# Optimization experiments

Hardware: AMD Instinct MI355X
Metric: run time of the kernel (lower is better)

## Reference

```python
import jax, jax.numpy as jnp
import numpy as np

SCALE_DTYPE = jnp.float32

def rotate_half(x):
    half = x.shape[-1] // 2
    return jnp.concatenate([-x[..., half:], x[..., :half]], axis=-1)

def apply_rope(x, cos, sin):
    # x: [B,T,H,Dh]; cos/sin: [T,Dh] -> broadcast to [1,T,1,Dh]
    c = cos[None, :, None, :]
    s = sin[None, :, None, :]
    return x * c + rotate_half(x) * s

def setup_inputs() -> dict:
    key = jax.random.key(0)
    ks = jax.random.split(key, 7)
    B, T, D, H, Dh = 4, 2048, 1024, 16, 64
    x = jax.random.normal(ks[0], (B, T, D), dtype=jnp.float32)
    cos = jax.random.uniform(ks[1], (T, Dh), dtype=jnp.float32)
    sin = jax.random.uniform(ks[2], (T, Dh), dtype=jnp.float32)
    scale = 1.0 / np.sqrt(D)
    Wq = jax.random.normal(ks[3], (D, D), dtype=jnp.float32) * scale
    Wk = jax.random.normal(ks[4], (D, D), dtype=jnp.float32) * scale
    Wv = jax.random.normal(ks[5], (D, D), dtype=jnp.float32) * scale
    Wo = jax.random.normal(ks[6], (D, D), dtype=jnp.float32) * scale
    return {"x": x, "cos": cos, "sin": sin, "Wq": Wq, "Wk": Wk, "Wv": Wv, "Wo": Wo}

def reference(x, cos, sin, Wq, Wk, Wv, Wo):
    B, T, D = x.shape
    H, Dh = 16, 64
    # Linear projections (weights stored [in, out]) and split heads
    q = (x @ Wq).reshape(B, T, H, Dh)
    k = (x @ Wk).reshape(B, T, H, Dh)
    v = (x @ Wv).reshape(B, T, H, Dh)
    q = apply_rope(q, cos[:T], sin[:T])
    k = apply_rope(k, cos[:T], sin[:T])
    scale = 1.0 / jnp.sqrt(jnp.asarray(Dh, dtype=x.dtype))
    # [B,H,T,T] causal scores
    scores = jnp.einsum('bthd,bshd->bhts', q, k) * scale
    causal = jnp.tril(jnp.ones((T, T), dtype=bool))
    scores = jnp.where(causal[None, None, :, :], scores, jnp.asarray(-jnp.inf, dtype=scores.dtype))
    weights = jax.nn.softmax(scores, axis=-1)
    out = jnp.einsum('bhts,bshd->bthd', weights, v).reshape(B, T, D)
    return out @ Wo
```

## Files before the change

kernel.cpp:

```cpp
#include <hip/hip_runtime.h>
#include <cstdint>
#include <cstddef>

typedef unsigned short ushort_t;
typedef __attribute__((ext_vector_type(8))) short short8;
typedef __attribute__((ext_vector_type(4))) float float4v;
typedef __attribute__((ext_vector_type(4))) unsigned short ushort4v;

__device__ __forceinline__ float b2f(ushort_t u) {
    uint32_t x = ((uint32_t)u) << 16;
    float f;
    __builtin_memcpy(&f, &x, 4);
    return f;
}
__device__ __forceinline__ ushort_t f2b(float f) {
    uint32_t x;
    __builtin_memcpy(&x, &f, 4);
    uint32_t r = (x + 0x7fffu + ((x >> 16) & 1u)) >> 16;
    return (ushort_t)r;
}
__device__ __forceinline__ ushort_t f2b_trunc(float f) {
    uint32_t x;
    __builtin_memcpy(&x, &f, 4);
    return (ushort_t)(x >> 16);
}

typedef __attribute__((address_space(3))) void lds_void;
typedef __attribute__((address_space(1))) const void gbl_void;
__device__ __forceinline__ void gload16(const void* g, void* l) {
    __builtin_amdgcn_global_load_lds((gbl_void*)(uintptr_t)g, (lds_void*)(uintptr_t)l, 16, 0, 0);
}

__global__ void detect_dtype(const ushort_t* __restrict__ cosp, int* __restrict__ flag) {
    int tid = threadIdx.x;
    int bad = 0;
    for (int i = tid; i < 512; i += 64) {
        ushort_t u = cosp[i];
        int sign = u >> 15;
        int e = (u >> 7) & 0xFF;
        if (sign || e > 126) bad = 1;
    }
    int anybad = __any(bad);
    if (tid == 0) *flag = anybad ? 1 : 0;
}

__global__ __launch_bounds__(256) void convert_x(const void* __restrict__ in,
                                                 ushort_t* __restrict__ out,
                                                 const int* __restrict__ flag) {
    if (*flag == 0) return;
    int i = (blockIdx.x * 256 + threadIdx.x) * 4;
    float4v v = *(const float4v*)((const float*)in + i);
    ushort4v o;
#pragma unroll
    for (int j = 0; j < 4; ++j) o[j] = f2b(v[j]);
    *(ushort4v*)(out + i) = o;
}

__global__ __launch_bounds__(256) void convert_cs(const void* __restrict__ c,
                                                  const void* __restrict__ s,
                                                  ushort_t* __restrict__ cb,
                                                  ushort_t* __restrict__ sb,
                                                  const int* __restrict__ flag) {
    int f = *flag;
    int i = blockIdx.x * 256 + threadIdx.x;
    if (i >= 131072) return;
    if (f) {
        cb[i] = f2b(((const float*)c)[i]);
        sb[i] = f2b(((const float*)s)[i]);
    } else {
        cb[i] = ((const ushort_t*)c)[i];
        sb[i] = ((const ushort_t*)s)[i];
    }
}

__global__ __launch_bounds__(256) void transpose_w4(const void* __restrict__ w0,
                                                    const void* __restrict__ w1,
                                                    const void* __restrict__ w2,
                                                    const void* __restrict__ w3,
                                                    ushort_t* __restrict__ out,
                                                    const int* __restrict__ flag) {
    int f = *flag;
    int z = blockIdx.z;
    const void* in = (z == 0) ? w0 : (z == 1) ? w1 : (z == 2) ? w2 : w3;
    ushort_t* o = out + (size_t)z * 1024 * 1024;
    __shared__ ushort_t tile[32][33];
    int bx = blockIdx.x * 32;
    int by = blockIdx.y * 32;
    int tx = threadIdx.x & 31;
    int ty = threadIdx.x >> 5;
    for (int r = ty; r < 32; r += 8) {
        size_t idx = (size_t)(by + r) * 1024 + bx + tx;
        tile[r][tx] = f ? f2b(((const float*)in)[idx]) : ((const ushort_t*)in)[idx];
    }
    __syncthreads();
    for (int r = ty; r < 32; r += 8)
        o[(size_t)(bx + r) * 1024 + by + tx] = tile[tx][r];
}

template <int W>
__device__ __forceinline__ void vm_wait() {
    if constexpr (W == 6)      asm volatile("s_waitcnt vmcnt(6)" ::: "memory");
    else                       asm volatile("s_waitcnt vmcnt(0)" ::: "memory");
}
#define KBAR()                                       \
    do {                                             \
        asm volatile("" ::: "memory");               \
        __builtin_amdgcn_s_barrier();                \
        asm volatile("" ::: "memory");               \
    } while (0)

__global__ __launch_bounds__(512, 2) void gemm_qkv(const ushort_t* __restrict__ X0,
                                                   const ushort_t* __restrict__ X1,
                                                   const ushort_t* __restrict__ Wt,
                                                   ushort_t* __restrict__ qk,
                                                   ushort_t* __restrict__ vt,
                                                   const ushort_t* __restrict__ cosb,
                                                   const ushort_t* __restrict__ sinb,
                                                   const int* __restrict__ flagp) {
    __shared__ ushort_t LDS[73728];
    char* LDSc = (char*)LDS;

    int tid = threadIdx.x;
    int lane = tid & 63;
    int wave = tid >> 6;
    int wm = wave >> 1;
    int wn = wave & 1;
    int quad = lane >> 4;
    int l16 = lane & 15;

    int id = blockIdx.x;
    int xcd = id & 7;
    int r = id >> 3;
    int m0 = (r & 31) * 256;
    int n0 = (xcd * 3 + (r >> 5)) * 128;

    const ushort_t* Xb = (*flagp) ? X1 : X0;

    int lrow = lane >> 3;
    int lslot = (lane & 7) ^ lrow;
    const ushort_t* aSrc = Xb + (size_t)(m0 + wave * 32 + lrow) * 1024 + lslot * 8;
    const ushort_t* bSrc = Wt + (size_t)(n0 + wave * 16 + lrow) * 1024 + lslot * 8;
    int ldsA_w = (wave * 32) * 128;
    int ldsB_w = (wave * 16) * 128;

    int aoff0 = (wm * 64 + l16) * 128 + ((quad ^ (l16 & 7)) * 16);
    int aoff1 = (wm * 64 + l16) * 128 + (((4 + quad) ^ (l16 & 7)) * 16);
    int boff0 = (wn * 64 + l16) * 128 + ((quad ^ (l16 & 7)) * 16);
    int boff1 = (wn * 64 + l16) * 128 + (((4 + quad) ^ (l16 & 7)) * 16);

    float4v acc[4][4];
#pragma unroll
    for (int i = 0; i < 4; ++i)
#pragma unroll
        for (int n = 0; n < 4; ++n) acc[i][n] = (float4v){0.f, 0.f, 0.f, 0.f};

#define STAGE6(t, jj)                                                       \
    do {                                                                    \
        const ushort_t* as_ = aSrc + (jj) * 64;                             \
        const ushort_t* bs_ = bSrc + (jj) * 64;                             \
        char* al_ = LDSc + (t) * 32768 + ldsA_w;                            \
        char* bl_ = LDSc + 98304 + (t) * 16384 + ldsB_w;                    \
        gload16(as_, al_);                                                  \
        gload16(as_ + 8 * 1024, al_ + 1024);                                \
        gload16(as_ + 16 * 1024, al_ + 2048);                               \
        gload16(as_ + 24 * 1024, al_ + 3072);                               \
        gload16(bs_, bl_);                                                  \
        gload16(bs_ + 8 * 1024, bl_ + 1024);                                \
    } while (0)

#define COMPUTE(t)                                                          \
    do {                                                                    \
        const char* ab_ = LDSc + (t) * 32768;                               \
        const char* bb_ = LDSc + 98304 + (t) * 16384;                       \
        short8 a0_[4], b0_[4], a1_[4], b1_[4];                              \
        _Pragma("unroll") for (int i = 0; i < 4; ++i) {                     \
            a0_[i] = *(const short8*)(ab_ + aoff0 + i * 2048);              \
            a1_[i] = *(const short8*)(ab_ + aoff1 + i * 2048);              \
        }                                                                   \
        _Pragma("unroll") for (int n = 0; n < 4; ++n) {                     \
            b0_[n] = *(const short8*)(bb_ + boff0 + n * 2048);              \
            b1_[n] = *(const short8*)(bb_ + boff1 + n * 2048);              \
        }                                                                   \
        __builtin_amdgcn_s_setprio(1);                                      \
        _Pragma("unroll") for (int i = 0; i < 4; ++i)                       \
            _Pragma("unroll") for (int n = 0; n < 4; ++n)                   \
                acc[i][n] = __builtin_amdgcn_mfma_f32_16x16x32_bf16(        \
                    a0_[i], b0_[n], acc[i][n], 0, 0, 0);                    \
        _Pragma("unroll") for (int i = 0; i < 4; ++i)                       \
            _Pragma("unroll") for (int n = 0; n < 4; ++n)                   \
                acc[i][n] = __builtin_amdgcn_mfma_f32_16x16x32_bf16(        \
                    a1_[i], b1_[n], acc[i][n], 0, 0, 0);                    \
        __builtin_amdgcn_s_setprio(0);                                      \
    } while (0)

    STAGE6(0, 0);
    STAGE6(1, 1);
    vm_wait<6>();
    KBAR();

#pragma unroll 1
    for (int g = 0; g < 4; ++g) {
        int j = g * 3;
        STAGE6(2, j + 2);
        COMPUTE(0);
        vm_wait<6>();
        KBAR();
        STAGE6(0, j + 3);
        COMPUTE(1);
        vm_wait<6>();
        KBAR();
        STAGE6(1, j + 4);
        COMPUTE(2);
        vm_wait<6>();
        KBAR();
    }
    STAGE6(2, 14);
    COMPUTE(0);
    vm_wait<6>();
    KBAR();
    STAGE6(0, 15);
    COMPUTE(1);
    vm_wait<6>();
    KBAR();
    COMPUTE(2);
    vm_wait<0>();
    KBAR();
    COMPUTE(0);

#undef STAGE6
#undef COMPUTE

    int nglob = n0 + wn * 64;
    int region = nglob >> 10;
    int hcol = (nglob & 1023) >> 6;

    if (region < 2) {
        int colbase = region * 1024 + hcol * 64 + l16;
#pragma unroll
        for (int i = 0; i < 4; ++i) {
            int rowb = m0 + wm * 64 + i * 16 + quad * 4;
#pragma unroll
            for (int rr = 0; rr < 4; ++rr) {
                int row = rowb + rr;
                int t = row & 2047;
                const ushort_t* cp = cosb + t * 64 + l16;
                const ushort_t* sp = sinb + t * 64 + l16;
                float c0 = b2f(cp[0]), c1 = b2f(cp[16]), c2 = b2f(cp[32]), c3 = b2f(cp[48]);
                float s0v = b2f(sp[0]), s1v = b2f(sp[16]), s2v = b2f(sp[32]), s3v = b2f(sp[48]);
                float a0 = acc[i][0][rr], a1 = acc[i][1][rr], a2 = acc[i][2][rr], a3 = acc[i][3][rr];
                float o0 = a0 * c0 - a2 * s0v;
                float o1 = a1 * c1 - a3 * s1v;
                float o2 = a2 * c2 + a0 * s2v;
                float o3 = a3 * c3 + a1 * s3v;
                size_t base = (size_t)row * 2048 + colbase;
                qk[base] = f2b(o0);
                qk[base + 16] = f2b(o1);
                qk[base + 32] = f2b(o2);
                qk[base + 48] = f2b(o3);
            }
        }
    } else {
#pragma unroll
        for (int i = 0; i < 4; ++i) {
            int rowb = m0 + wm * 64 + i * 16 + quad * 4;
            int b = rowb >> 11;
            int t0 = rowb & 2047;
            size_t hb = (size_t)(b * 16 + hcol) * 64;
#pragma unroll
            for (int n = 0; n < 4; ++n) {
                int d = l16 + n * 16;
                ushort4v pk;
#pragma unroll
                for (int rr = 0; rr < 4; ++rr) pk[rr] = f2b(acc[i][n][rr]);
                *(ushort4v*)(vt + (hb + d) * 2048 + t0) = pk;
            }
        }
    }
}

__global__ __launch_bounds__(256) void gemm_proj(const ushort_t* __restrict__ A, int lda,
                                                 const ushort_t* __restrict__ Bt,
                                                 void* __restrict__ C, int ldc,
                                                 int K,
                                                 const int* __restrict__ flagp) {
    __shared__ ushort_t Al[128 * 64];
    __shared__ ushort_t Bl[128 * 64];

    int tid = threadIdx.x;
    int lane = tid & 63;
    int wave = tid >> 6;
    int wr = wave >> 1;
    int wc = wave & 1;
    int quad = lane >> 4;
    int l16 = lane & 15;

    int id = blockIdx.x;
    int m0 = (id >> 3) * 128;
    int n0 = (id & 7) * 128;

    int lrow = lane >> 3;
    int lcol = (lane & 7) * 8;

    float4v acc[4][4];
#pragma unroll
    for (int i = 0; i < 4; ++i)
#pragma unroll
        for (int j = 0; j < 4; ++j) acc[i][j] = (float4v){0.f, 0.f, 0.f, 0.f};

    for (int k0 = 0; k0 < K; k0 += 64) {
        __syncthreads();
#pragma unroll
        for (int p = 0; p < 4; ++p) {
            int row = wave * 32 + p * 8 + lrow;
            gload16(A + (size_t)(m0 + row) * lda + k0 + lcol, &Al[(size_t)(wave * 4 + p) * 512]);
            gload16(Bt + (size_t)(n0 + row) * K + k0 + lcol, &Bl[(size_t)(wave * 4 + p) * 512]);
        }
        __syncthreads();

#pragma unroll
        for (int ks = 0; ks < 2; ++ks) {
            int kf = ks * 32 + quad * 8;
            short8 a_frag[4], b_frag[4];
#pragma unroll
            for (int i = 0; i < 4; ++i) {
                a_frag[i] = *(const short8*)(&Al[(wr * 64 + i * 16 + l16) * 64 + kf]);
                b_frag[i] = *(const short8*)(&Bl[(wc * 64 + i * 16 + l16) * 64 + kf]);
            }
#pragma unroll
            for (int i = 0; i < 4; ++i)
#pragma unroll
                for (int j = 0; j < 4; ++j)
                    acc[i][j] = __builtin_amdgcn_mfma_f32_16x16x32_bf16(
                        a_frag[i], b_frag[j], acc[i][j], 0, 0, 0);
        }
    }

    int f32out = *flagp;

#pragma unroll
    for (int i = 0; i < 4; ++i) {
        int rowb = m0 + wr * 64 + i * 16 + quad * 4;
#pragma unroll
        for (int r = 0; r < 4; ++r) {
            size_t base = (size_t)(rowb + r) * ldc + n0 + wc * 64 + l16;
            if (f32out) {
                float* Cf = (float*)C;
#pragma unroll
                for (int j = 0; j < 4; ++j) Cf[base + j * 16] = acc[i][j][r];
            } else {
                ushort_t* Cb = (ushort_t*)C;
#pragma unroll
                for (int j = 0; j < 4; ++j) Cb[base + j * 16] = f2b(acc[i][j][r]);
            }
        }
    }
}

__global__ __launch_bounds__(512, 4) void attn_mfma(ushort_t* qk,
                                                    const ushort_t* __restrict__ vt) {
    __shared__ ushort_t Kl[64 * 72];
    __shared__ ushort_t Vl[64 * 72];
    __shared__ ushort_t Pl[8 * 16 * 72];

    int tid = threadIdx.x;
    int lane = tid & 63;
    int wave = tid >> 6;
    int quad = lane >> 4;
    int l16 = lane & 15;

    int bxi = blockIdx.x;
    int bh = blockIdx.y;
    int b = bh >> 4;
    int h = bh & 15;

    ushort_t* Pw = &Pl[wave * 16 * 72];
    int rr = tid >> 3;
    int cc = (tid & 7) * 8;

    const float SCL = 0.125f * 1.44269504f;
    const float SMAX2 = 20.0f * 1.44269504f;

#pragma unroll 1
    for (int phase = 0; phase < 2; ++phase) {
        int qt = phase ? bxi : (15 - bxi);
        int row0 = qt * 128 + wave * 16;
        size_t qbase = ((size_t)(b * 2048 + row0)) * 2048 + h * 64;

        short8 qf[2];
        {
            const ushort_t* p = qk + qbase + (size_t)l16 * 2048 + quad * 8;
            qf[0] = *(const short8*)p;
            qf[1] = *(const short8*)(p + 32);
        }

        float4v oacc[4];
#pragma unroll
        for (int nt = 0; nt < 4; ++nt) oacc[nt] = (float4v){0.f, 0.f, 0.f, 0.f};
        float psum[4];
#pragma unroll
        for (int r = 0; r < 4; ++r) psum[r] = 0.f;

        int ntiles = 2 * qt + 2;

        short8 kreg, vreg;
        kreg = *(const short8*)(qk + ((size_t)(b * 2048 + rr)) * 2048 + 1024 + h * 64 + cc);
        vreg = *(const short8*)(vt + ((size_t)(bh * 64 + rr)) * 2048 + cc);

        for (int st = 0; st < ntiles; ++st) {
            int s0 = st * 64;
            __syncthreads();
            *(short8*)(&Kl[rr * 72 + cc]) = kreg;
            *(short8*)(&Vl[rr * 72 + cc]) = vreg;
            __syncthreads();

            if (st + 1 < ntiles) {
                int s1 = s0 + 64;
                kreg = *(const short8*)(qk + ((size_t)(b * 2048 + s1 + rr)) * 2048 + 1024 + h * 64 + cc);
                vreg = *(const short8*)(vt + ((size_t)(bh * 64 + rr)) * 2048 + s1 + cc);
            }

            if (s0 <= row0 + 15) {
                float4v sacc[4];
#pragma unroll
                for (int ct = 0; ct < 4; ++ct) sacc[ct] = (float4v){0.f, 0.f, 0.f, 0.f};
#pragma unroll
                for (int ks = 0; ks < 2; ++ks) {
                    short8 bfr[4];
#pragma unroll
                    for (int ct = 0; ct < 4; ++ct)
                        bfr[ct] = *(const short8*)(&Kl[(ct * 16 + l16) * 72 + ks * 32 + quad * 8]);
#pragma unroll
                    for (int ct = 0; ct < 4; ++ct)
                        sacc[ct] = __builtin_amdgcn_mfma_f32_16x16x32_bf16(
                            qf[ks], bfr[ct], sacc[ct], 0, 0, 0);
                }

                if ((s0 + 63) > row0) {
#pragma unroll
                    for (int r = 0; r < 4; ++r) {
                        int trow = row0 + quad * 4 + r;
                        float ps = 0.f;
#pragma unroll
                        for (int ct = 0; ct < 4; ++ct) {
                            float p = exp2f(sacc[ct][r] * SCL - SMAX2);
                            if ((s0 + ct * 16 + l16) > trow) p = 0.f;
                            ps += p;
                            Pw[(quad * 4 + r) * 72 + ct * 16 + l16] = f2b_trunc(p);
                        }
                        psum[r] += ps;
                    }
                } else {
#pragma unroll
                    for (int r = 0; r < 4; ++r) {
                        float ps = 0.f;
#pragma unroll
                        for (int ct = 0; ct < 4; ++ct) {
                            float p = exp2f(sacc[ct][r] * SCL - SMAX2);
                            ps += p;
                            Pw[(quad * 4 + r) * 72 + ct * 16 + l16] = f2b_trunc(p);
                        }
                        psum[r] += ps;
                    }
                }

#pragma unroll
                for (int ks = 0; ks < 2; ++ks) {
                    short8 bfr[4];
#pragma unroll
                    for (int nt = 0; nt < 4; ++nt)
                        bfr[nt] = *(const short8*)(&Vl[(nt * 16 + l16) * 72 + ks * 32 + quad * 8]);
                    short8 af = *(const short8*)(&Pw[l16 * 72 + ks * 32 + quad * 8]);
#pragma unroll
                    for (int nt = 0; nt < 4; ++nt)
                        oacc[nt] = __builtin_amdgcn_mfma_f32_16x16x32_bf16(
                            af, bfr[nt], oacc[nt], 0, 0, 0);
                }
            }
        }

#pragma unroll
        for (int r = 0; r < 4; ++r) {
            float ps = psum[r];
#pragma unroll
            for (int off = 1; off < 16; off <<= 1) ps += __shfl_xor(ps, off);
            float inv = 1.0f / ps;
            size_t base = qbase + (size_t)(quad * 4 + r) * 2048;
#pragma unroll
            for (int nt = 0; nt < 4; ++nt)
                qk[base + nt * 16 + l16] = f2b(oacc[nt][r] * inv);
        }
    }
}

extern "C" void kernel_launch(void* const* d_in, const int* in_sizes, int n_in,
                              void* d_out, int out_size, void* d_ws, size_t ws_size,
                              hipStream_t stream) {
    const void* x = d_in[0];
    const void* cosp = d_in[1];
    const void* sinp = d_in[2];
    const void* Wq = d_in[3];
    const void* Wk = d_in[4];
    const void* Wv = d_in[5];
    const void* Wo = d_in[6];

    char* ws = (char*)d_ws;
    int* flag = (int*)ws;
    ushort_t* vtg = (ushort_t*)(ws + 256);
    ushort_t* qk = vtg + (size_t)8192 * 2048;
    ushort_t* WT = qk + (size_t)8192 * 2048;
    ushort_t* WoT = WT + (size_t)3 * 1024 * 1024;
    ushort_t* cosb = WT + (size_t)4 * 1024 * 1024;
    ushort_t* sinb = cosb + (size_t)2048 * 64;
    ushort_t* xb = sinb + (size_t)2048 * 64;

    detect_dtype<<<1, 64, 0, stream>>>((const ushort_t*)cosp, flag);
    convert_cs<<<512, 256, 0, stream>>>(cosp, sinp, cosb, sinb, flag);
    convert_x<<<8192, 256, 0, stream>>>(x, xb, flag);
    transpose_w4<<<dim3(32, 32, 4), 256, 0, stream>>>(Wq, Wk, Wv, Wo, WT, flag);

    gemm_qkv<<<768, 512, 0, stream>>>((const ushort_t*)x, xb, WT, qk, vtg, cosb, sinb, flag);

    attn_mfma<<<dim3(8, 64), 512, 0, stream>>>(qk, vtg);

    gemm_proj<<<512, 256, 0, stream>>>(qk, 2048, WoT, d_out, 1024, 1024, flag);
}
```

Measured before the change: 291.3 us.

## Double-buffer attention K/V via direct LDS loads with swizzle; fold softmax scale into Q

The attention kernel now issues direct global-to-LDS loads into double-buffered, XOR-swizzled K/V tiles, replacing register staging into padded LDS. Each tile iteration needs one wait and barrier instead of two `__syncthreads`, and the next tile's load overlaps the current tile's compute. The softmax scale times log2(e) is folded into the Q projection epilogue, which removes a multiply and the constant max-offset subtraction before each exp2. Dropping that fixed offset raises overflow risk if scores get large, and scaling Q before bf16 rounding slightly changes numerics.

After: 281.8 us. 1.03x faster.

```diff
diff --git a/kernel.cpp b/kernel.cpp
--- a/kernel.cpp
+++ b/kernel.cpp
@@ -235,6 +235,7 @@
     int hcol = (nglob & 1023) >> 6;
 
     if (region < 2) {
+        float scl = (region == 0) ? 0.18033688f : 1.0f;
         int colbase = region * 1024 + hcol * 64 + l16;
 #pragma unroll
         for (int i = 0; i < 4; ++i) {
@@ -248,10 +249,10 @@
                 float c0 = b2f(cp[0]), c1 = b2f(cp[16]), c2 = b2f(cp[32]), c3 = b2f(cp[48]);
                 float s0v = b2f(sp[0]), s1v = b2f(sp[16]), s2v = b2f(sp[32]), s3v = b2f(sp[48]);
                 float a0 = acc[i][0][rr], a1 = acc[i][1][rr], a2 = acc[i][2][rr], a3 = acc[i][3][rr];
-                float o0 = a0 * c0 - a2 * s0v;
-                float o1 = a1 * c1 - a3 * s1v;
-                float o2 = a2 * c2 + a0 * s2v;
-                float o3 = a3 * c3 + a1 * s3v;
+                float o0 = (a0 * c0 - a2 * s0v) * scl;
+                float o1 = (a1 * c1 - a3 * s1v) * scl;
+                float o2 = (a2 * c2 + a0 * s2v) * scl;
+                float o3 = (a3 * c3 + a1 * s3v) * scl;
                 size_t base = (size_t)row * 2048 + colbase;
                 qk[base] = f2b(o0);
                 qk[base + 16] = f2b(o1);
@@ -358,8 +359,8 @@
 
 __global__ __launch_bounds__(512, 4) void attn_mfma(ushort_t* qk,
                                                     const ushort_t* __restrict__ vt) {
-    __shared__ ushort_t Kl[64 * 72];
-    __shared__ ushort_t Vl[64 * 72];
+    __shared__ ushort_t Kl[2][4096];
+    __shared__ ushort_t Vl[2][4096];
     __shared__ ushort_t Pl[8 * 16 * 72];
 
     int tid = threadIdx.x;
@@ -374,11 +375,15 @@
     int h = bh & 15;
 
     ushort_t* Pw = &Pl[wave * 16 * 72];
+
     int rr = tid >> 3;
-    int cc = (tid & 7) * 8;
-
-    const float SCL = 0.125f * 1.44269504f;
-    const float SMAX2 = 20.0f * 1.44269504f;
+    int sl = (tid & 7) ^ (rr & 7);
+    const ushort_t* ksrc = qk + (size_t)(b * 2048 + rr) * 2048 + 1024 + h * 64 + sl * 8;
+    const ushort_t* vsrc = vt + (size_t)(bh * 64 + rr) * 2048 + sl * 8;
+    char* kdst = (char*)&Kl[0][0] + wave * 1024;
+    char* vdst = (char*)&Vl[0][0] + wave * 1024;
+
+    int swr = l16 & 7;
 
 #pragma unroll 1
     for (int phase = 0; phase < 2; ++phase) {
@@ -402,24 +407,24 @@
 
         int ntiles = 2 * qt + 2;
 
-        short8 kreg, vreg;
-        kreg = *(const short8*)(qk + ((size_t)(b * 2048 + rr)) * 2048 + 1024 + h * 64 + cc);
-        vreg = *(const short8*)(vt + ((size_t)(bh * 64 + rr)) * 2048 + cc);
+        gload16(ksrc, kdst);
+        gload16(vsrc, vdst);
+        vm_wait<0>();
+        KBAR();
 
         for (int st = 0; st < ntiles; ++st) {
             int s0 = st * 64;
-            __syncthreads();
-            *(short8*)(&Kl[rr * 72 + cc]) = kreg;
-            *(short8*)(&Vl[rr * 72 + cc]) = vreg;
-            __syncthreads();
+            int buf = st & 1;
 
             if (st + 1 < ntiles) {
-                int s1 = s0 + 64;
-                kreg = *(const short8*)(qk + ((size_t)(b * 2048 + s1 + rr)) * 2048 + 1024 + h * 64 + cc);
-                vreg = *(const short8*)(vt + ((size_t)(bh * 64 + rr)) * 2048 + s1 + cc);
+                gload16(ksrc + (size_t)(s0 + 64) * 2048, kdst + ((st + 1) & 1) * 8192);
+                gload16(vsrc + (s0 + 64), vdst + ((st + 1) & 1) * 8192);
             }
 
             if (s0 <= row0 + 15) {
+                const char* kb = (const char*)&Kl[buf][0];
+                const char* vb = (const char*)&Vl[buf][0];
+
                 float4v sacc[4];
 #pragma unroll
                 for (int ct = 0; ct < 4; ++ct) sacc[ct] = (float4v){0.f, 0.f, 0.f, 0.f};
@@ -428,7 +433,8 @@
                     short8 bfr[4];
 #pragma unroll
                     for (int ct = 0; ct < 4; ++ct)
-                        bfr[ct] = *(const short8*)(&Kl[(ct * 16 + l16) * 72 + ks * 32 + quad * 8]);
+                        bfr[ct] = *(const short8*)(kb + (ct * 16 + l16) * 128 +
+                                                   (((ks * 4 + quad) ^ swr) * 16));
 #pragma unroll
                     for (int ct = 0; ct < 4; ++ct)
                         sacc[ct] = __builtin_amdgcn_mfma_f32_16x16x32_bf16(
@@ -442,7 +448,7 @@
                         float ps = 0.f;
 #pragma unroll
                         for (int ct = 0; ct < 4; ++ct) {
-                            float p = exp2f(sacc[ct][r] * SCL - SMAX2);
+                            float p = exp2f(sacc[ct][r]);
                             if ((s0 + ct * 16 + l16) > trow) p = 0.f;
                             ps += p;
                             Pw[(quad * 4 + r) * 72 + ct * 16 + l16] = f2b_trunc(p);
@@ -455,7 +461,7 @@
                         float ps = 0.f;
 #pragma unroll
                         for (int ct = 0; ct < 4; ++ct) {
-                            float p = exp2f(sacc[ct][r] * SCL - SMAX2);
+                            float p = exp2f(sacc[ct][r]);
                             ps += p;
                             Pw[(quad * 4 + r) * 72 + ct * 16 + l16] = f2b_trunc(p);
                         }
@@ -468,7 +474,8 @@
                     short8 bfr[4];
 #pragma unroll
                     for (int nt = 0; nt < 4; ++nt)
-                        bfr[nt] = *(const short8*)(&Vl[(nt * 16 + l16) * 72 + ks * 32 + quad * 8]);
+                        bfr[nt] = *(const short8*)(vb + (nt * 16 + l16) * 128 +
+                                                   (((ks * 4 + quad) ^ swr) * 16));
                     short8 af = *(const short8*)(&Pw[l16 * 72 + ks * 32 + quad * 8]);
 #pragma unroll
                     for (int nt = 0; nt < 4; ++nt)
@@ -476,6 +483,9 @@
                             af, bfr[nt], oacc[nt], 0, 0, 0);
                 }
             }
+
+            vm_wait<0>();
+            KBAR();
         }
 
 #pragma unroll
```
